# Kernel tuning notes

Measured on AMD Instinct MI355X. Metric: run time of the kernel, lower is better.

## Reference

```python
import jax, jax.numpy as jnp
import numpy as np

N, K, D, A = 65536, 1024, 256, 64  # batch, n_clusters, s_dim, a_dim
STD_0 = 1.0


@jax.custom_vjp
def grad1abs(x):
    # torch Grad1Abs: forward = |x|, backward flips sign only where x < 0
    # (so grad at exactly 0 is +1, unlike jnp.abs).
    return jnp.abs(x)


def _g1a_fwd(x):
    return jnp.abs(x), x


def _g1a_bwd(x, g):
    return (jnp.where(x < 0, -g, g),)


grad1abs.defvjp(_g1a_fwd, _g1a_bwd)


def setup_inputs() -> dict:
    key = jax.random.key(0)
    k_s, k_c, k_w, k_m = jax.random.split(key, 4)
    return {
        "s": jax.random.normal(k_s, (N, D), dtype=jnp.float32),
        "centers": jax.random.normal(k_c, (K, D), dtype=jnp.float32),
        "c_weights": jax.random.normal(k_w, (K,), dtype=jnp.float32),
        "means": jax.random.normal(k_m, (K, A), dtype=jnp.float32),
        "log_sigma": jnp.full((A,), np.log(STD_0), dtype=jnp.float32),
        "log_temp": jnp.float32(0.0),
    }


def reference(s, centers, c_weights, means, log_sigma, log_temp):
    # squared euclidean distance to centers, computed as a GEMM-friendly
    # expansion of sum((s[:,None,:] - centers[None,:,:])**2, -1): [N, K]
    sq_dist = (
        jnp.sum(s * s, axis=-1, keepdims=True)          # [N, 1]
        + jnp.sum(centers * centers, axis=-1)[None, :]  # [1, K]
        - 2.0 * s @ centers.T                           # [N, K]
    )
    # unnormalized membership: |c_weights| * exp(-exp(log_temp) * dist)
    w = grad1abs(c_weights)[None, :] * jnp.exp(-jnp.exp(log_temp) * sq_dist)
    # normalize with +1 in the denominator (soft "none of the clusters" mass)
    w = w / (jnp.sum(w, axis=-1, keepdims=True) + 1.0)
    mean = w @ means                      # [N, A]
    chol = jnp.diag(jnp.exp(log_sigma))   # [A, A]
    return mean, chol
```

## Files before the change

kernel.cpp:

```cpp
#include <hip/hip_runtime.h>

#define N_ROWS 65536
#define K_CL   1024
#define D_DIM  256
#define A_DIM  64
#define CHUNK  32
#define NCH    (K_CL / CHUNK)
#define CB     4096

#define WS_Q_OFF (128 * 1024)

typedef float    f32x4  __attribute__((ext_vector_type(4)));
typedef int      i32x8  __attribute__((ext_vector_type(8)));
typedef unsigned u32x4  __attribute__((ext_vector_type(4)));

#define UNIT_SCALE 0x7F7F7F7F

__device__ __forceinline__ unsigned f2e4m3(float f) {
    unsigned u = __builtin_bit_cast(unsigned, f);
    unsigned sg = (u >> 24) & 0x80u;
    int e8 = (int)((u >> 23) & 0xFF) - 120;
    unsigned m = u & 0x7FFFFFu;
    if (e8 <= 0) return sg;
    unsigned r = m + 0x7FFFFu + ((m >> 20) & 1u);
    m = r >> 20;
    if (m == 8u) { m = 0u; e8 += 1; }
    return sg | ((unsigned)e8 << 3) | m;
}
__device__ __forceinline__ unsigned pack4_fp8(f32x4 v) {
    return f2e4m3(v.x) | (f2e4m3(v.y) << 8) | (f2e4m3(v.z) << 16) | (f2e4m3(v.w) << 24);
}
__device__ __forceinline__ unsigned f2e2m1(float x) {
    const float ax = fabsf(x);
    unsigned c = (ax > 0.25f) + (ax > 0.75f) + (ax > 1.25f) + (ax > 1.75f)
               + (ax > 2.5f) + (ax > 3.5f) + (ax > 5.0f);
    return c | (x < 0.f ? 8u : 0u);
}

__global__ __launch_bounds__(256) void prep_kernel(const float* __restrict__ centers,
                                                   const float* __restrict__ cw,
                                                   const float* __restrict__ log_temp,
                                                   unsigned char* __restrict__ ws)
{
    const int tid = threadIdx.x, lane = tid & 63, wid = tid >> 6;
    const float te = __expf(log_temp[0]) * 1.44269504088896340736f;
    #pragma unroll
    for (int i = 0; i < 4; ++i) {
        const int row = blockIdx.x * 16 + wid * 4 + i;
        const f32x4 v = ((const f32x4*)(centers + (long)row * D_DIM))[lane];
        float ss = v.x * v.x + v.y * v.y + v.z * v.z + v.w * v.w;
        #pragma unroll
        for (int m = 1; m < 64; m <<= 1) ss += __shfl_xor(ss, m, 64);
        if (lane == 0)
            ((float*)(ws + WS_Q_OFF))[row] = fmaf(-te, ss, __log2f(fabsf(cw[row])));
    }
    const int tg = blockIdx.x * 256 + tid;
    if (tg < 8192) {
        const int c    = tg >> 8;
        const int rest = tg & 255;
        const int t    = rest >> 7;
        const int ks   = (rest >> 6) & 1;
        const int l    = rest & 63;
        const int col  = c * CHUNK + t * 16 + (l & 15);
        const int kb   = ks * 128 + (l >> 4) * 32;
        const float* cp = centers + (long)col * D_DIM + kb;
        unsigned wd[4];
        #pragma unroll
        for (int d = 0; d < 4; ++d) {
            unsigned acc = 0;
            #pragma unroll
            for (int j = 0; j < 8; ++j)
                acc |= f2e2m1(cp[8 * d + j]) << (4 * j);
            wd[d] = acc;
        }
        *(u32x4*)(ws + (long)tg * 16) = (u32x4){wd[0], wd[1], wd[2], wd[3]};
    }
}

__device__ __attribute__((noinline))
void slow_path(const float* s, const float* centers, const float* cw, const float* means,
               float temp, long row0, int nrows, int lane, float* out)
{
    for (int r2 = 0; r2 < nrows; ++r2) {
        const long row = row0 + r2;
        const float4 sv = ((const float4*)(s + row * D_DIM))[lane];
        float acc_a = 0.f, rsum = 0.f;
        for (int k = 0; k < K_CL; ++k) {
            const float4 cv = ((const float4*)(centers + (long)k * D_DIM))[lane];
            float d2 = (sv.x - cv.x) * (sv.x - cv.x) + (sv.y - cv.y) * (sv.y - cv.y)
                     + (sv.z - cv.z) * (sv.z - cv.z) + (sv.w - cv.w) * (sv.w - cv.w);
            #pragma unroll
            for (int m = 1; m < 64; m <<= 1) d2 += __shfl_xor(d2, m, 64);
            const float w = fabsf(cw[k]) * __expf(-temp * d2);
            rsum += w;
            acc_a += w * means[k * A_DIM + lane];
        }
        out[row * A_DIM + lane] = acc_a / (rsum + 1.f);
    }
}

__global__ __launch_bounds__(64, 4)
void fused_kernel(const float* __restrict__ s,
                  const unsigned char* __restrict__ ws,
                  const float* __restrict__ means,
                  const float* __restrict__ centers,
                  const float* __restrict__ cw,
                  const float* __restrict__ log_temp,
                  float* __restrict__ out)
{
    const int lane = threadIdx.x & 63;
    const int lo   = lane & 15;
    const int hi   = lane >> 4;
    const long brow0 = (long)blockIdx.x * 16;
    const int cbase = blockIdx.x & (NCH - 1);

    const float temp = __expf(log_temp[0]);
    const float te   = temp * 1.44269504088896340736f;
    const float t2e  = 2.0f * te;

    const float* qptr = (const float*)(ws + WS_Q_OFF);

    i32x8 bbA[4], bbB[4];
    float qA0, qA1, qB0, qB1;

#define LOADB(BB, ci) do {                                                               \
        const unsigned char* _g = ws + (ci) * CB + (lane << 4);                          \
        _Pragma("unroll")                                                                \
        for (int _m = 0; _m < 4; ++_m) {                                                 \
            const u32x4 _v = *(const u32x4*)(_g + _m * 1024);                            \
            BB[_m] = (i32x8){(int)_v.x, (int)_v.y, (int)_v.z, (int)_v.w, 0, 0, 0, 0};    \
        }                                                                                \
    } while (0)

    {
        const int ci0 = cbase;
        const int ci1 = (cbase + 1) & (NCH - 1);
        LOADB(bbA, ci0); qA0 = qptr[ci0 * CHUNK + lo]; qA1 = qptr[ci0 * CHUNK + 16 + lo];
        LOADB(bbB, ci1); qB0 = qptr[ci1 * CHUNK + lo]; qB1 = qptr[ci1 * CHUNK + 16 + lo];
    }

    i32x8 af[2];
    float ss = 0.f;
    {
        const float* srow = s + (brow0 + lo) * D_DIM;
        #pragma unroll
        for (int sl = 0; sl < 2; ++sl) {
            const float* p = srow + sl * 128 + hi * 32;
            unsigned w[8];
            #pragma unroll
            for (int i = 0; i < 4; ++i) {
                const f32x4 u = *(const f32x4*)(p + i * 8);
                const f32x4 v = *(const f32x4*)(p + i * 8 + 4);
                ss += u.x * u.x + u.y * u.y + u.z * u.z + u.w * u.w;
                ss += v.x * v.x + v.y * v.y + v.z * v.z + v.w * v.w;
#if __has_builtin(__builtin_amdgcn_cvt_pk_fp8_f32)
                unsigned d0 = (unsigned)__builtin_amdgcn_cvt_pk_fp8_f32(u.x, u.y, 0, false);
                d0 = (unsigned)__builtin_amdgcn_cvt_pk_fp8_f32(u.z, u.w, (int)d0, true);
                unsigned d1 = (unsigned)__builtin_amdgcn_cvt_pk_fp8_f32(v.x, v.y, 0, false);
                d1 = (unsigned)__builtin_amdgcn_cvt_pk_fp8_f32(v.z, v.w, (int)d1, true);
#else
                unsigned d0 = pack4_fp8(u), d1 = pack4_fp8(v);
#endif
                w[2 * i] = d0; w[2 * i + 1] = d1;
            }
            af[sl] = (i32x8){(int)w[0], (int)w[1], (int)w[2], (int)w[3],
                             (int)w[4], (int)w[5], (int)w[6], (int)w[7]};
        }
        ss += __shfl_xor(ss, 16, 64);
        ss += __shfl_xor(ss, 32, 64);
    }
    float a1[4];
    #pragma unroll
    for (int r = 0; r < 4; ++r)
        a1[r] = -te * __shfl(ss, hi * 4 + r, 64);

    float amax = -1e30f;

#define STEP(BB, Q0, Q1, cc, PF) do {                                                    \
        f32x4 a0a = {0.f, 0.f, 0.f, 0.f};                                                \
        f32x4 a0b = {0.f, 0.f, 0.f, 0.f};                                                \
        f32x4 a1a = {0.f, 0.f, 0.f, 0.f};                                                \
        f32x4 a1b = {0.f, 0.f, 0.f, 0.f};                                                \
        a0a = __builtin_amdgcn_mfma_scale_f32_16x16x128_f8f6f4(                          \
                  af[0], BB[0], a0a, 0, 4, 0, UNIT_SCALE, 0, UNIT_SCALE);                \
        a0b = __builtin_amdgcn_mfma_scale_f32_16x16x128_f8f6f4(                          \
                  af[1], BB[1], a0b, 0, 4, 0, UNIT_SCALE, 0, UNIT_SCALE);                \
        a1a = __builtin_amdgcn_mfma_scale_f32_16x16x128_f8f6f4(                          \
                  af[0], BB[2], a1a, 0, 4, 0, UNIT_SCALE, 0, UNIT_SCALE);                \
        a1b = __builtin_amdgcn_mfma_scale_f32_16x16x128_f8f6f4(                          \
                  af[1], BB[3], a1b, 0, 4, 0, UNIT_SCALE, 0, UNIT_SCALE);                \
        const float _cq0 = Q0, _cq1 = Q1;                                                \
        if (PF) {               \
            const int _ci = (cbase + (cc) + 2) & (NCH - 1);                              \
            LOADB(BB, _ci);                                                              \
            Q0 = qptr[_ci * CHUNK + lo];                                                 \
            Q1 = qptr[_ci * CHUNK + 16 + lo];                                            \
        }                                                                                \
        float _g0[4], _g1[4];                                                            \
        _Pragma("unroll")                                                                \
        for (int _r = 0; _r < 4; ++_r) {                                                 \
            _g0[_r] = fmaf(t2e, a0a[_r], fmaf(t2e, a0b[_r], a1[_r]));                    \
            _g1[_r] = fmaf(t2e, a1a[_r], fmaf(t2e, a1b[_r], a1[_r]));                    \
        }                                                                                \
        const float _m0 = fmaxf(fmaxf(_g0[0], _g0[1]), fmaxf(_g0[2], _g0[3]));           \
        const float _m1 = fmaxf(fmaxf(_g1[0], _g1[1]), fmaxf(_g1[2], _g1[3]));           \
        amax = fmaxf(amax, fmaxf(_m0 + _cq0, _m1 + _cq1));                               \
    } while (0)

    #pragma unroll 1
    for (int c2 = 0; c2 < NCH - 4; c2 += 2) {
        STEP(bbA, qA0, qA1, c2, 1);
        STEP(bbB, qB0, qB1, c2 + 1, 1);
    }
    STEP(bbA, qA0, qA1, NCH - 4, 1);
    STEP(bbB, qB0, qB1, NCH - 3, 1);
    STEP(bbA, qA0, qA1, NCH - 2, 0);
    STEP(bbB, qB0, qB1, NCH - 1, 0);
#undef STEP
#undef LOADB

    const unsigned long long bal = __ballot(amax > -150.0f);
    if (bal != 0ULL) {
        slow_path(s, centers, cw, means, temp, brow0, 16, lane, out);
    } else {
        const float4 z = {0.f, 0.f, 0.f, 0.f};
        float4* ob = (float4*)(out + brow0 * A_DIM);
        #pragma unroll
        for (int i = 0; i < 4; ++i) ob[lane + 64 * i] = z;
    }
}

__global__ void chol_kernel(const float* __restrict__ log_sigma, float* __restrict__ out2)
{
    const int i = blockIdx.x * 256 + threadIdx.x;
    const int r = i >> 6, c = i & 63;
    out2[i] = (r == c) ? __expf(log_sigma[r]) : 0.0f;
}

extern "C" void kernel_launch(void* const* d_in, const int* in_sizes, int n_in,
                              void* d_out, int out_size, void* d_ws, size_t ws_size,
                              hipStream_t stream)
{
    const float* s       = (const float*)d_in[0];
    const float* centers = (const float*)d_in[1];
    const float* cwts    = (const float*)d_in[2];
    const float* means   = (const float*)d_in[3];
    const float* lsig    = (const float*)d_in[4];
    const float* ltemp   = (const float*)d_in[5];
    float* out = (float*)d_out;
    unsigned char* ws = (unsigned char*)d_ws;

    prep_kernel<<<64, 256, 0, stream>>>(centers, cwts, ltemp, ws);
    fused_kernel<<<N_ROWS / 16, 64, 0, stream>>>(s, ws, means, centers, cwts, ltemp, out);
    chol_kernel<<<(A_DIM * A_DIM) / 256, 256, 0, stream>>>(lsig, out + (long)N_ROWS * A_DIM);
}
```

Baseline: 41.16 us.

## Pre-quantize s to fp8 in a separate kernel before fused pass

Adds a prep_s_kernel that converts each 16-row tile of s to fp8 MFMA operand layout and precomputes the scaled row norms into workspace. The main kernel then loads the prepacked fp8 operands and norms instead of reading fp32 s and converting it inline. The goal is to take conversion work and fp32 traffic out of the MFMA loop. The cost is an extra launch and an extra full pass over s, plus roughly 16 MB of workspace writes and reads. The old path is kept as a fallback when the workspace is too small.

Result: slower. 49.57 us (+20.4%).

```diff
diff --git a/kernel.cpp b/kernel.cpp
--- a/kernel.cpp
+++ b/kernel.cpp
@@ -8,7 +8,10 @@
 #define NCH    (K_CL / CHUNK)
 #define CB     4096
 
-#define WS_Q_OFF (128 * 1024)
+#define WS_Q_OFF   (128 * 1024)
+#define WS_S_OFF   (132 * 1024)
+#define WS_A1_OFF  (WS_S_OFF + (long)N_ROWS * D_DIM)
+#define WS_NEEDED  ((size_t)(WS_A1_OFF + (long)N_ROWS * 4))
 
 typedef float    f32x4  __attribute__((ext_vector_type(4)));
 typedef int      i32x8  __attribute__((ext_vector_type(8)));
@@ -35,6 +38,17 @@
     unsigned c = (ax > 0.25f) + (ax > 0.75f) + (ax > 1.25f) + (ax > 1.75f)
                + (ax > 2.5f) + (ax > 3.5f) + (ax > 5.0f);
     return c | (x < 0.f ? 8u : 0u);
+}
+__device__ __forceinline__ unsigned cvt8(f32x4 u, f32x4 v, unsigned& d0, unsigned& d1) {
+#if __has_builtin(__builtin_amdgcn_cvt_pk_fp8_f32)
+    d0 = (unsigned)__builtin_amdgcn_cvt_pk_fp8_f32(u.x, u.y, 0, false);
+    d0 = (unsigned)__builtin_amdgcn_cvt_pk_fp8_f32(u.z, u.w, (int)d0, true);
+    d1 = (unsigned)__builtin_amdgcn_cvt_pk_fp8_f32(v.x, v.y, 0, false);
+    d1 = (unsigned)__builtin_amdgcn_cvt_pk_fp8_f32(v.z, v.w, (int)d1, true);
+#else
+    d0 = pack4_fp8(u); d1 = pack4_fp8(v);
+#endif
+    return d0;
 }
 
 __global__ __launch_bounds__(256) void prep_kernel(const float* __restrict__ centers,
@@ -75,6 +89,44 @@
         }
         *(u32x4*)(ws + (long)tg * 16) = (u32x4){wd[0], wd[1], wd[2], wd[3]};
     }
+}
+
+__global__ __launch_bounds__(256) void prep_s_kernel(const float* __restrict__ s,
+                                                     const float* __restrict__ log_temp,
+                                                     unsigned char* __restrict__ ws)
+{
+    const int tid  = threadIdx.x;
+    const int lane = tid & 63;
+    const int wid  = tid >> 6;
+    const int lo   = lane & 15;
+    const int hi   = lane >> 4;
+    const int rb   = blockIdx.x * 4 + wid;
+    const float te = __expf(log_temp[0]) * 1.44269504088896340736f;
+
+    const float* srow = s + ((long)rb * 16 + lo) * D_DIM;
+    float ss = 0.f;
+    #pragma unroll
+    for (int sl = 0; sl < 2; ++sl) {
+        const float* p = srow + sl * 128 + hi * 32;
+        unsigned w[8];
+        #pragma unroll
+        for (int i = 0; i < 4; ++i) {
+            const f32x4 u = *(const f32x4*)(p + i * 8);
+            const f32x4 v = *(const f32x4*)(p + i * 8 + 4);
+            ss += u.x * u.x + u.y * u.y + u.z * u.z + u.w * u.w;
+            ss += v.x * v.x + v.y * v.y + v.z * v.z + v.w * v.w;
+            unsigned d0, d1;
+            cvt8(u, v, d0, d1);
+            w[2 * i] = d0; w[2 * i + 1] = d1;
+        }
+        const i32x8 af = {(int)w[0], (int)w[1], (int)w[2], (int)w[3],
+                          (int)w[4], (int)w[5], (int)w[6], (int)w[7]};
+        *(i32x8*)(ws + WS_S_OFF + ((long)rb * 2 + sl) * 2048 + lane * 32) = af;
+    }
+    ss += __shfl_xor(ss, 16, 64);
+    ss += __shfl_xor(ss, 32, 64);
+    if (hi == 0)
+        ((float*)(ws + WS_A1_OFF))[rb * 16 + lo] = -te * ss;
 }
 
 __device__ __attribute__((noinline))
@@ -100,13 +152,13 @@
 }
 
 __global__ __launch_bounds__(64, 4)
-void fused_kernel(const float* __restrict__ s,
-                  const unsigned char* __restrict__ ws,
-                  const float* __restrict__ means,
-                  const float* __restrict__ centers,
-                  const float* __restrict__ cw,
-                  const float* __restrict__ log_temp,
-                  float* __restrict__ out)
+void fused_lean(const float* __restrict__ s,
+                const unsigned char* __restrict__ ws,
+                const float* __restrict__ means,
+                const float* __restrict__ centers,
+                const float* __restrict__ cw,
+                const float* __restrict__ log_temp,
+                float* __restrict__ out)
 {
     const int lane = threadIdx.x & 63;
     const int lo   = lane & 15;
@@ -140,39 +192,17 @@
     }
 
     i32x8 af[2];
-    float ss = 0.f;
     {
-        const float* srow = s + (brow0 + lo) * D_DIM;
-        #pragma unroll
-        for (int sl = 0; sl < 2; ++sl) {
-            const float* p = srow + sl * 128 + hi * 32;
-            unsigned w[8];
-            #pragma unroll
-            for (int i = 0; i < 4; ++i) {
-                const f32x4 u = *(const f32x4*)(p + i * 8);
-                const f32x4 v = *(const f32x4*)(p + i * 8 + 4);
-                ss += u.x * u.x + u.y * u.y + u.z * u.z + u.w * u.w;
-                ss += v.x * v.x + v.y * v.y + v.z * v.z + v.w * v.w;
-#if __has_builtin(__builtin_amdgcn_cvt_pk_fp8_f32)
-                unsigned d0 = (unsigned)__builtin_amdgcn_cvt_pk_fp8_f32(u.x, u.y, 0, false);
-                d0 = (unsigned)__builtin_amdgcn_cvt_pk_fp8_f32(u.z, u.w, (int)d0, true);
-                unsigned d1 = (unsigned)__builtin_amdgcn_cvt_pk_fp8_f32(v.x, v.y, 0, false);
-                d1 = (unsigned)__builtin_amdgcn_cvt_pk_fp8_f32(v.z, v.w, (int)d1, true);
-#else
-                unsigned d0 = pack4_fp8(u), d1 = pack4_fp8(v);
-#endif
-                w[2 * i] = d0; w[2 * i + 1] = d1;
-            }
-            af[sl] = (i32x8){(int)w[0], (int)w[1], (int)w[2], (int)w[3],
-                             (int)w[4], (int)w[5], (int)w[6], (int)w[7]};
-        }
-        ss += __shfl_xor(ss, 16, 64);
-        ss += __shfl_xor(ss, 32, 64);
+        const unsigned char* sbase = ws + WS_S_OFF + (long)blockIdx.x * 4096;
+        af[0] = *(const i32x8*)(sbase + lane * 32);
+        af[1] = *(const i32x8*)(sbase + 2048 + lane * 32);
     }
     float a1[4];
-    #pragma unroll
-    for (int r = 0; r < 4; ++r)
-        a1[r] = -te * __shfl(ss, hi * 4 + r, 64);
+    {
+        const float* a1t = (const float*)(ws + WS_A1_OFF) + brow0;
+        #pragma unroll
+        for (int r = 0; r < 4; ++r) a1[r] = a1t[hi * 4 + r];
+    }
 
     float amax = -1e30f;
 
@@ -190,7 +220,132 @@
         a1b = __builtin_amdgcn_mfma_scale_f32_16x16x128_f8f6f4(                          \
                   af[1], BB[3], a1b, 0, 4, 0, UNIT_SCALE, 0, UNIT_SCALE);                \
         const float _cq0 = Q0, _cq1 = Q1;                                                \
-        if (PF) {               \
+        if (PF) {                                                                        \
+            const int _ci = (cbase + (cc) + 2) & (NCH - 1);                              \
+            LOADB(BB, _ci);                                                              \
+            Q0 = qptr[_ci * CHUNK + lo];                                                 \
+            Q1 = qptr[_ci * CHUNK + 16 + lo];                                            \
+        }                                                                                \
+        float _g0[4], _g1[4];                                                            \
+        _Pragma("unroll")                                                                \
+        for (int _r = 0; _r < 4; ++_r) {                                                 \
+            _g0[_r] = fmaf(t2e, a0a[_r], fmaf(t2e, a0b[_r], a1[_r]));                    \
+            _g1[_r] = fmaf(t2e, a1a[_r], fmaf(t2e, a1b[_r], a1[_r]));                    \
+        }                                                                                \
+        const float _m0 = fmaxf(fmaxf(_g0[0], _g0[1]), fmaxf(_g0[2], _g0[3]));           \
+        const float _m1 = fmaxf(fmaxf(_g1[0], _g1[1]), fmaxf(_g1[2], _g1[3]));           \
+        amax = fmaxf(amax, fmaxf(_m0 + _cq0, _m1 + _cq1));                               \
+    } while (0)
+
+    #pragma unroll 1
+    for (int c2 = 0; c2 < NCH - 4; c2 += 2) {
+        STEP(bbA, qA0, qA1, c2, 1);
+        STEP(bbB, qB0, qB1, c2 + 1, 1);
+    }
+    STEP(bbA, qA0, qA1, NCH - 4, 1);
+    STEP(bbB, qB0, qB1, NCH - 3, 1);
+    STEP(bbA, qA0, qA1, NCH - 2, 0);
+    STEP(bbB, qB0, qB1, NCH - 1, 0);
+#undef STEP
+#undef LOADB
+
+    const unsigned long long bal = __ballot(amax > -150.0f);
+    if (bal != 0ULL) {
+        slow_path(s, centers, cw, means, temp, brow0, 16, lane, out);
+    } else {
+        const float4 z = {0.f, 0.f, 0.f, 0.f};
+        float4* ob = (float4*)(out + brow0 * A_DIM);
+        #pragma unroll
+        for (int i = 0; i < 4; ++i) ob[lane + 64 * i] = z;
+    }
+}
+
+__global__ __launch_bounds__(64, 4)
+void fused_r15(const float* __restrict__ s,
+               const unsigned char* __restrict__ ws,
+               const float* __restrict__ means,
+               const float* __restrict__ centers,
+               const float* __restrict__ cw,
+               const float* __restrict__ log_temp,
+               float* __restrict__ out)
+{
+    const int lane = threadIdx.x & 63;
+    const int lo   = lane & 15;
+    const int hi   = lane >> 4;
+    const long brow0 = (long)blockIdx.x * 16;
+    const int cbase = blockIdx.x & (NCH - 1);
+
+    const float temp = __expf(log_temp[0]);
+    const float te   = temp * 1.44269504088896340736f;
+    const float t2e  = 2.0f * te;
+
+    const float* qptr = (const float*)(ws + WS_Q_OFF);
+
+    i32x8 bbA[4], bbB[4];
+    float qA0, qA1, qB0, qB1;
+
+#define LOADB(BB, ci) do {                                                               \
+        const unsigned char* _g = ws + (ci) * CB + (lane << 4);                          \
+        _Pragma("unroll")                                                                \
+        for (int _m = 0; _m < 4; ++_m) {                                                 \
+            const u32x4 _v = *(const u32x4*)(_g + _m * 1024);                            \
+            BB[_m] = (i32x8){(int)_v.x, (int)_v.y, (int)_v.z, (int)_v.w, 0, 0, 0, 0};    \
+        }                                                                                \
+    } while (0)
+
+    {
+        const int ci0 = cbase;
+        const int ci1 = (cbase + 1) & (NCH - 1);
+        LOADB(bbA, ci0); qA0 = qptr[ci0 * CHUNK + lo]; qA1 = qptr[ci0 * CHUNK + 16 + lo];
+        LOADB(bbB, ci1); qB0 = qptr[ci1 * CHUNK + lo]; qB1 = qptr[ci1 * CHUNK + 16 + lo];
+    }
+
+    i32x8 af[2];
+    float ss = 0.f;
+    {
+        const float* srow = s + (brow0 + lo) * D_DIM;
+        #pragma unroll
+        for (int sl = 0; sl < 2; ++sl) {
+            const float* p = srow + sl * 128 + hi * 32;
+            unsigned w[8];
+            #pragma unroll
+            for (int i = 0; i < 4; ++i) {
+                const f32x4 u = *(const f32x4*)(p + i * 8);
+                const f32x4 v = *(const f32x4*)(p + i * 8 + 4);
+                ss += u.x * u.x + u.y * u.y + u.z * u.z + u.w * u.w;
+                ss += v.x * v.x + v.y * v.y + v.z * v.z + v.w * v.w;
+                unsigned d0, d1;
+                cvt8(u, v, d0, d1);
+                w[2 * i] = d0; w[2 * i + 1] = d1;
+            }
+            af[sl] = (i32x8){(int)w[0], (int)w[1], (int)w[2], (int)w[3],
+                             (int)w[4], (int)w[5], (int)w[6], (int)w[7]};
+        }
+        ss += __shfl_xor(ss, 16, 64);
+        ss += __shfl_xor(ss, 32, 64);
+    }
+    float a1[4];
+    #pragma unroll
+    for (int r = 0; r < 4; ++r)
+        a1[r] = -te * __shfl(ss, hi * 4 + r, 64);
+
+    float amax = -1e30f;
+
+#define STEP(BB, Q0, Q1, cc, PF) do {                                                    \
+        f32x4 a0a = {0.f, 0.f, 0.f, 0.f};                                                \
+        f32x4 a0b = {0.f, 0.f, 0.f, 0.f};                                                \
+        f32x4 a1a = {0.f, 0.f, 0.f, 0.f};                                                \
+        f32x4 a1b = {0.f, 0.f, 0.f, 0.f};                                                \
+        a0a = __builtin_amdgcn_mfma_scale_f32_16x16x128_f8f6f4(                          \
+                  af[0], BB[0], a0a, 0, 4, 0, UNIT_SCALE, 0, UNIT_SCALE);                \
+        a0b = __builtin_amdgcn_mfma_scale_f32_16x16x128_f8f6f4(                          \
+                  af[1], BB[1], a0b, 0, 4, 0, UNIT_SCALE, 0, UNIT_SCALE);                \
+        a1a = __builtin_amdgcn_mfma_scale_f32_16x16x128_f8f6f4(                          \
+                  af[0], BB[2], a1a, 0, 4, 0, UNIT_SCALE, 0, UNIT_SCALE);                \
+        a1b = __builtin_amdgcn_mfma_scale_f32_16x16x128_f8f6f4(                          \
+                  af[1], BB[3], a1b, 0, 4, 0, UNIT_SCALE, 0, UNIT_SCALE);                \
+        const float _cq0 = Q0, _cq1 = Q1;                                                \
+        if (PF) {                                                                        \
             const int _ci = (cbase + (cc) + 2) & (NCH - 1);                              \
             LOADB(BB, _ci);                                                              \
             Q0 = qptr[_ci * CHUNK + lo];                                                 \
@@ -251,6 +406,11 @@
     unsigned char* ws = (unsigned char*)d_ws;
 
     prep_kernel<<<64, 256, 0, stream>>>(centers, cwts, ltemp, ws);
-    fused_kernel<<<N_ROWS / 16, 64, 0, stream>>>(s, ws, means, centers, cwts, ltemp, out);
+    if (ws_size >= WS_NEEDED) {
+        prep_s_kernel<<<1024, 256, 0, stream>>>(s, ltemp, ws);
+        fused_lean<<<N_ROWS / 16, 64, 0, stream>>>(s, ws, means, centers, cwts, ltemp, out);
+    } else {
+        fused_r15<<<N_ROWS / 16, 64, 0, stream>>>(s, ws, means, centers, cwts, ltemp, out);
+    }
     chol_kernel<<<(A_DIM * A_DIM) / 256, 256, 0, stream>>>(lsig, out + (long)N_ROWS * A_DIM);
 }
```
